# Kernel optimization log

Hardware: AMD Instinct MI355X
Metric: run time of the kernel (lower is better)

Reference implementation:

```python
import jax, jax.numpy as jnp
import numpy as np
from jax import lax

C = 256
HEADS = 8
HEAD_DIM = C // HEADS
B, H, W = 16, 32, 32
EPS = 1e-5


def conv3x3(x, w, b):
    # x: [B,C,H,W], w: [O,I,3,3]
    y = lax.conv_general_dilated(x, w, (1, 1), 'SAME',
                                 dimension_numbers=('NCHW', 'OIHW', 'NCHW'))
    return y + b[None, :, None, None]


def conv1x1(x, w, b):
    # w: [O,C]; pointwise conv as einsum
    return jnp.einsum('oc,bchw->bohw', w, x) + b[None, :, None, None]


def batchnorm(x, gamma, beta, mean, var):
    inv = gamma / jnp.sqrt(var + EPS)
    return x * inv[None, :, None, None] + (beta - mean * inv)[None, :, None, None]


def setup_inputs() -> dict:
    key = jax.random.key(0)
    ks = jax.random.split(key, 16)
    s3 = 1.0 / np.sqrt(C * 9)
    s1 = 1.0 / np.sqrt(C)
    return {
        'x': jax.random.normal(ks[0], (B, C, H, W), jnp.float32),
        'conv1_w': jax.random.normal(ks[1], (C, C, 3, 3), jnp.float32) * s3,
        'conv1_b': jnp.zeros((C,), jnp.float32),
        'bn1_gamma': jnp.ones((C,), jnp.float32),
        'bn1_beta': jnp.zeros((C,), jnp.float32),
        'bn1_mean': jax.random.normal(ks[2], (C,), jnp.float32) * 0.1,
        'bn1_var': jax.random.uniform(ks[3], (C,), jnp.float32, 0.5, 1.5),
        'conv2_w': jax.random.normal(ks[4], (C, C, 3, 3), jnp.float32) * s3,
        'conv2_b': jnp.zeros((C,), jnp.float32),
        'bn2_gamma': jnp.ones((C,), jnp.float32),
        'bn2_beta': jnp.zeros((C,), jnp.float32),
        'bn2_mean': jax.random.normal(ks[5], (C,), jnp.float32) * 0.1,
        'bn2_var': jax.random.uniform(ks[6], (C,), jnp.float32, 0.5, 1.5),
        'q_w': jax.random.normal(ks[7], (C, C), jnp.float32) * s1,
        'q_b': jnp.zeros((C,), jnp.float32),
        'k_w': jax.random.normal(ks[8], (C, C), jnp.float32) * s1,
        'k_b': jnp.zeros((C,), jnp.float32),
        'v_w': jax.random.normal(ks[9], (C, C), jnp.float32) * s1,
        'v_b': jnp.zeros((C,), jnp.float32),
        'out_w': jax.random.normal(ks[10], (C, C), jnp.float32) * s1,
        'out_b': jnp.zeros((C,), jnp.float32),
        'gate': jnp.asarray(0.1, jnp.float32),
    }


def reference(x, conv1_w, conv1_b, bn1_gamma, bn1_beta, bn1_mean, bn1_var,
              conv2_w, conv2_b, bn2_gamma, bn2_beta, bn2_mean, bn2_var,
              q_w, q_b, k_w, k_b, v_w, v_b, out_w, out_b, gate):
    b, c, h, w = x.shape
    n = h * w
    residual = x
    # conv residual path
    conv_out = jax.nn.relu(batchnorm(conv3x3(x, conv1_w, conv1_b),
                                     bn1_gamma, bn1_beta, bn1_mean, bn1_var))
    conv_out = batchnorm(conv3x3(conv_out, conv2_w, conv2_b),
                         bn2_gamma, bn2_beta, bn2_mean, bn2_var)
    # spatial multi-head attention (eval mode: dropout is identity)
    q = conv1x1(x, q_w, q_b).reshape(b, HEADS, HEAD_DIM, n)
    k = conv1x1(x, k_w, k_b).reshape(b, HEADS, HEAD_DIM, n)
    v = conv1x1(x, v_w, v_b).reshape(b, HEADS, HEAD_DIM, n)
    scores = jnp.einsum('bhdn,bhdm->bhnm', q, k) / np.sqrt(HEAD_DIM).astype(np.float32)
    attn = jax.nn.softmax(scores, axis=-1)  # [B,heads,N,N]
    attn_out = jnp.einsum('bhdm,bhnm->bhdn', v, attn).reshape(b, c, h, w)
    attn_out = conv1x1(attn_out, out_w, out_b)
    out = conv_out + jax.nn.sigmoid(gate) * attn_out + residual
    return jax.nn.relu(out)
```

## Files before the change

### kernel.cpp

```cpp
#include <hip/hip_runtime.h>
#include <hip/hip_bf16.h>

using bf16 = __hip_bfloat16;
typedef __attribute__((ext_vector_type(4))) float floatx4;
typedef __attribute__((ext_vector_type(8))) __bf16 bf16x8;
typedef __attribute__((ext_vector_type(4))) __bf16 bf16x4;
typedef __attribute__((ext_vector_type(8))) unsigned short ushort8;

__device__ __forceinline__ void prep_one(const float* __restrict__ src,
                                         bf16* __restrict__ dst, int idx, int ntaps)
{
    const int kk = idx & 31, o = (idx >> 5) & 255, kc = (idx >> 13) & 7, t = idx >> 16;
    dst[idx] = __float2bfloat16(src[(o * 256 + kc * 32 + kk) * ntaps + t]);
}

__global__ __launch_bounds__(256) void prep_all(
    const float* __restrict__ x,
    const float* __restrict__ w1, const float* __restrict__ w2,
    const float* __restrict__ qw, const float* __restrict__ kw,
    const float* __restrict__ vw, const float* __restrict__ ow,
    bf16* __restrict__ xT, bf16* __restrict__ w1f, bf16* __restrict__ w2f,
    bf16* __restrict__ qwf, bf16* __restrict__ kwf,
    bf16* __restrict__ vwf, bf16* __restrict__ owf)
{
    __shared__ float T[64][65];
    const int blk = blockIdx.x, tid = threadIdx.x;
    if (blk < 1024) {
        const int n0 = (blk & 15) * 64, c0 = ((blk >> 4) & 3) * 64, b = blk >> 6;
        #pragma unroll
        for (int it = 0; it < 4; ++it) {
            const int tau = tid + it * 256;
            const int c = tau >> 4, seg = tau & 15;
            const float4 vv = *(const float4*)&x[((b * 256 + c0 + c) << 10) + n0 + seg * 4];
            T[seg * 4 + 0][c] = vv.x; T[seg * 4 + 1][c] = vv.y;
            T[seg * 4 + 2][c] = vv.z; T[seg * 4 + 3][c] = vv.w;
        }
        __syncthreads();
        #pragma unroll
        for (int it = 0; it < 2; ++it) {
            const int tau = tid + it * 256;
            const int n = tau >> 3, seg = tau & 7;
            bf16x8 o8;
            #pragma unroll
            for (int q = 0; q < 8; ++q) o8[q] = (__bf16)T[n][seg * 8 + q];
            *(bf16x8*)&xT[(((b << 10) + n0 + n) << 8) + c0 + seg * 8] = o8;
        }
    } else if (blk < 2176) {
        const int base = (blk - 1024) * 256 + tid;
        #pragma unroll
        for (int k = 0; k < 4; ++k) {
            const int idx = base + k * 294912;
            if (idx < 589824) prep_one(w1, w1f, idx, 9);
            else              prep_one(w2, w2f, idx - 589824, 9);
        }
    } else {
        const int r = (blk - 2176) * 256 + tid;
        prep_one(qw, qwf, r, 1);
        prep_one(kw, kwf, r, 1);
        prep_one(vw, vwf, r, 1);
        prep_one(ow, owf, r, 1);
    }
}

template<int MODE, int NTAPS>
__global__ __launch_bounds__(256) void gemm_k(
    const bf16* __restrict__ Wf, const bf16* __restrict__ Act,
    const float* __restrict__ bias,
    const float* __restrict__ gam, const float* __restrict__ bet,
    const float* __restrict__ mu, const float* __restrict__ var,
    const float* __restrict__ c2, const float* __restrict__ resid,
    const float* __restrict__ gate,
    void* __restrict__ outp)
{
    __shared__ __align__(16) bf16 smem[(NTAPS == 9) ? (6 * 34 * 40) : (128 * 40)];

    const int bn = blockIdx.x, bo = blockIdx.y, b = blockIdx.z;
    const int tid = threadIdx.x;
    const int wave = tid >> 6, lane = tid & 63;
    const int quad = lane >> 4, l16 = lane & 15;
    const int wm = wave & 1, wn = wave >> 1;

    floatx4 acc[4][2] = {};

    for (int kc = 0; kc < 8; ++kc) {
        const int kg = kc * 32;
        __syncthreads();
        if (NTAPS == 9) {
            #pragma unroll
            for (int it = 0; it < 4; ++it) {
                const int tau = tid + it * 256;
                if (tau < 816) {
                    const int pair = tau >> 2, kseg = tau & 3;
                    const int yi = pair / 34, x34 = pair - yi * 34;
                    const int gy = bn * 4 - 1 + yi, gx = x34 - 1;
                    ushort8 val = {0, 0, 0, 0, 0, 0, 0, 0};
                    if (gy >= 0 && gy < 32 && gx >= 0 && gx < 32)
                        val = *(const ushort8*)&Act[(((b << 10) + (gy << 5) + gx) << 8) + kg + kseg * 8];
                    *(ushort8*)&smem[((yi * 34 + x34) * 40) + kseg * 8] = val;
                }
            }
        } else {
            #pragma unroll
            for (int it = 0; it < 2; ++it) {
                const int tau = tid + it * 256;
                const int row = tau >> 2, kseg = tau & 3;
                *(ushort8*)&smem[row * 40 + kseg * 8] =
                    *(const ushort8*)&Act[(((b << 10) + bn * 128 + row) << 8) + kg + kseg * 8];
            }
        }
        __syncthreads();

        #pragma unroll
        for (int t = 0; t < NTAPS; ++t) {
            const int dy = (NTAPS == 9) ? (t / 3 - 1) : 0;
            const int dx = (NTAPS == 9) ? (t % 3 - 1) : 0;
            bf16x8 af[4], wf[2];
            #pragma unroll
            for (int p = 0; p < 4; ++p) {
                const int m = wm * 64 + p * 16 + l16;
                if (NTAPS == 9) {
                    const int y = m >> 5, xx = m & 31;
                    af[p] = *(const bf16x8*)&smem[(((y + 1 + dy) * 34 + (xx + 1 + dx)) * 40) + quad * 8];
                } else {
                    af[p] = *(const bf16x8*)&smem[m * 40 + quad * 8];
                }
            }
            #pragma unroll
            for (int p = 0; p < 2; ++p) {
                const int ocl = wn * 32 + p * 16 + l16;
                wf[p] = *(const bf16x8*)&Wf[((((t * 8 + kc) << 8) + bo * 64 + ocl) << 5) + quad * 8];
            }
            #pragma unroll
            for (int i = 0; i < 4; ++i)
                #pragma unroll
                for (int j = 0; j < 2; ++j)
                    acc[i][j] = __builtin_amdgcn_mfma_f32_16x16x32_bf16(af[i], wf[j], acc[i][j], 0, 0, 0);
        }
    }

    float sg = 0.0f;
    if (MODE == 2) sg = 1.0f / (1.0f + __expf(-gate[0]));

    if constexpr (MODE == 0) {
        #pragma unroll
        for (int i = 0; i < 4; ++i)
            #pragma unroll
            for (int r = 0; r < 4; ++r) {
                const int n = bn * 128 + wm * 64 + i * 16 + quad * 4 + r;
                #pragma unroll
                for (int j = 0; j < 2; ++j) {
                    const int oc = bo * 64 + wn * 32 + j * 16 + l16;
                    const float inv = gam[oc] * rsqrtf(var[oc] + 1e-5f);
                    const float v = (acc[i][j][r] + bias[oc]) * inv + (bet[oc] - mu[oc] * inv);
                    ((bf16*)outp)[(((b << 10) + n) << 8) + oc] =
                        __float2bfloat16(v < 0.0f ? 0.0f : v);
                }
            }
    } else {
        #pragma unroll
        for (int i = 0; i < 4; ++i) {
            const int n0 = bn * 128 + wm * 64 + i * 16 + quad * 4;
            #pragma unroll
            for (int j = 0; j < 2; ++j) {
                const int oc = bo * 64 + wn * 32 + j * 16 + l16;
                const int idx0 = ((b * 256 + oc) << 10) + n0;
                const float bs = bias[oc];
                float4 o;
                if constexpr (MODE == 1) {
                    const float inv = gam[oc] * rsqrtf(var[oc] + 1e-5f);
                    const float sh = bet[oc] - mu[oc] * inv;
                    o.x = (acc[i][j][0] + bs) * inv + sh;
                    o.y = (acc[i][j][1] + bs) * inv + sh;
                    o.z = (acc[i][j][2] + bs) * inv + sh;
                    o.w = (acc[i][j][3] + bs) * inv + sh;
                } else {
                    const float4 cc = *(const float4*)&c2[idx0];
                    const float4 rr = *(const float4*)&resid[idx0];
                    o.x = cc.x + sg * (acc[i][j][0] + bs) + rr.x;
                    o.y = cc.y + sg * (acc[i][j][1] + bs) + rr.y;
                    o.z = cc.z + sg * (acc[i][j][2] + bs) + rr.z;
                    o.w = cc.w + sg * (acc[i][j][3] + bs) + rr.w;
                    o.x = o.x < 0.0f ? 0.0f : o.x;
                    o.y = o.y < 0.0f ? 0.0f : o.y;
                    o.z = o.z < 0.0f ? 0.0f : o.z;
                    o.w = o.w < 0.0f ? 0.0f : o.w;
                }
                *(float4*)&((float*)outp)[idx0] = o;
            }
        }
    }
}

__global__ __launch_bounds__(256) void qkv_k(
    const bf16* __restrict__ Wq, const bf16* __restrict__ Wk, const bf16* __restrict__ Wv,
    const bf16* __restrict__ Act,
    const float* __restrict__ bq, const float* __restrict__ bk, const float* __restrict__ bv,
    bf16* __restrict__ Oq, bf16* __restrict__ Ok, bf16* __restrict__ Ov, float qscale)
{
    __shared__ __align__(16) bf16 smem[128 * 40];
    const int bn = blockIdx.x, by = blockIdx.y, b = blockIdx.z;
    const int sel = by >> 2, bo = by & 3;
    const bf16* __restrict__ Wf = (sel == 0) ? Wq : (sel == 1) ? Wk : Wv;
    const float* __restrict__ bias = (sel == 0) ? bq : (sel == 1) ? bk : bv;
    const float scale = (sel == 0) ? qscale : 1.0f;

    const int tid = threadIdx.x;
    const int wave = tid >> 6, lane = tid & 63;
    const int quad = lane >> 4, l16 = lane & 15;
    const int wm = wave & 1, wn = wave >> 1;

    floatx4 acc[4][2] = {};

    for (int kc = 0; kc < 8; ++kc) {
        const int kg = kc * 32;
        __syncthreads();
        #pragma unroll
        for (int it = 0; it < 2; ++it) {
            const int tau = tid + it * 256;
            const int row = tau >> 2, kseg = tau & 3;
            *(ushort8*)&smem[row * 40 + kseg * 8] =
                *(const ushort8*)&Act[(((b << 10) + bn * 128 + row) << 8) + kg + kseg * 8];
        }
        __syncthreads();

        bf16x8 af[4], wf[2];
        #pragma unroll
        for (int p = 0; p < 4; ++p)
            af[p] = *(const bf16x8*)&smem[(wm * 64 + p * 16 + l16) * 40 + quad * 8];
        #pragma unroll
        for (int p = 0; p < 2; ++p) {
            const int ocl = wn * 32 + p * 16 + l16;
            wf[p] = *(const bf16x8*)&Wf[(((kc << 8) + bo * 64 + ocl) << 5) + quad * 8];
        }
        #pragma unroll
        for (int i = 0; i < 4; ++i)
            #pragma unroll
            for (int j = 0; j < 2; ++j)
                acc[i][j] = __builtin_amdgcn_mfma_f32_16x16x32_bf16(af[i], wf[j], acc[i][j], 0, 0, 0);
    }

    if (sel < 2) {
        bf16* __restrict__ outp = (sel == 0) ? Oq : Ok;
        #pragma unroll
        for (int i = 0; i < 4; ++i)
            #pragma unroll
            for (int r = 0; r < 4; ++r) {
                const int n = bn * 128 + wm * 64 + i * 16 + quad * 4 + r;
                #pragma unroll
                for (int j = 0; j < 2; ++j) {
                    const int oc = bo * 64 + wn * 32 + j * 16 + l16;
                    outp[(((b << 10) + n) << 8) + oc] =
                        __float2bfloat16((acc[i][j][r] + bias[oc]) * scale);
                }
            }
    } else {
        #pragma unroll
        for (int i = 0; i < 4; ++i) {
            const int n0 = bn * 128 + wm * 64 + i * 16 + quad * 4;
            #pragma unroll
            for (int j = 0; j < 2; ++j) {
                const int oc = bo * 64 + wn * 32 + j * 16 + l16;
                const float bs = bias[oc];
                bf16x4 o4;
                #pragma unroll
                for (int r = 0; r < 4; ++r) o4[r] = (__bf16)(acc[i][j][r] + bs);
                *(bf16x4*)&Ov[((b * 256 + oc) << 10) + n0] = o4;
            }
        }
    }
}

__global__ __launch_bounds__(256) void attn_kernel(
    const bf16* __restrict__ Q, const bf16* __restrict__ K,
    const bf16* __restrict__ V, bf16* __restrict__ O)
{
    __shared__ __align__(16) bf16 Pl[4][32][136];

    const int qb = blockIdx.x, h = blockIdx.y, b = blockIdx.z;
    const int tid = threadIdx.x;
    const int wave = tid >> 6, lane = tid & 63;
    const int quad = lane >> 4, l16 = lane & 15;

    const int qrow0 = (b << 10) + qb * 128 + wave * 32;

    bf16x8 qf[2];
    #pragma unroll
    for (int i = 0; i < 2; ++i)
        qf[i] = *(const bf16x8*)&Q[((qrow0 + i * 16 + l16) << 8) + h * 32 + quad * 8];

    float lp[2] = {0.0f, 0.0f};
    floatx4 oacc[2][2] = {};

    for (int kt = 0; kt < 8; ++kt) {
        const int krow0 = (b << 10) + kt * 128;
        bf16x8 kf[8];
        #pragma unroll
        for (int kb = 0; kb < 8; ++kb)
            kf[kb] = *(const bf16x8*)&K[((krow0 + kb * 16 + l16) << 8) + h * 32 + quad * 8];
        bf16x8 vb[2][4];
        #pragma unroll
        for (int jd = 0; jd < 2; ++jd)
            #pragma unroll
            for (int kk = 0; kk < 4; ++kk)
                vb[jd][kk] = *(const bf16x8*)&V[((b * 256 + h * 32 + jd * 16 + l16) << 10)
                                               + kt * 128 + kk * 32 + quad * 8];

        #pragma unroll
        for (int kb = 0; kb < 8; ++kb) {
            #pragma unroll
            for (int i = 0; i < 2; ++i) {
                floatx4 zz = {0.f, 0.f, 0.f, 0.f};
                floatx4 st = __builtin_amdgcn_mfma_f32_16x16x32_bf16(kf[kb], qf[i], zz, 0, 0, 0);
                const float e0 = __expf(st[0]), e1 = __expf(st[1]);
                const float e2 = __expf(st[2]), e3 = __expf(st[3]);
                lp[i] += (e0 + e1) + (e2 + e3);
                bf16x4 p4 = {(__bf16)e0, (__bf16)e1, (__bf16)e2, (__bf16)e3};
                *(bf16x4*)&Pl[wave][i * 16 + l16][kb * 16 + quad * 4] = p4;
            }
        }

        #pragma unroll
        for (int kk = 0; kk < 4; ++kk) {
            bf16x8 pf[2];
            #pragma unroll
            for (int i = 0; i < 2; ++i)
                pf[i] = *(const bf16x8*)&Pl[wave][i * 16 + l16][kk * 32 + quad * 8];
            #pragma unroll
            for (int jd = 0; jd < 2; ++jd)
                #pragma unroll
                for (int i = 0; i < 2; ++i)
                    oacc[jd][i] = __builtin_amdgcn_mfma_f32_16x16x32_bf16(
                        vb[jd][kk], pf[i], oacc[jd][i], 0, 0, 0);
        }
    }

    #pragma unroll
    for (int i = 0; i < 2; ++i) {
        float l = lp[i];
        l += __shfl_xor(l, 16, 64);
        l += __shfl_xor(l, 32, 64);
        const float inv = 1.0f / l;
        const int qn = qrow0 + i * 16 + l16;
        #pragma unroll
        for (int jd = 0; jd < 2; ++jd) {
            bf16x4 o4;
            #pragma unroll
            for (int r = 0; r < 4; ++r) o4[r] = (__bf16)(oacc[jd][i][r] * inv);
            *(bf16x4*)&O[((qn) << 8) + h * 32 + jd * 16 + quad * 4] = o4;
        }
    }
}

extern "C" void kernel_launch(void* const* d_in, const int* in_sizes, int n_in,
                              void* d_out, int out_size, void* d_ws, size_t ws_size,
                              hipStream_t stream)
{
    const float* x    = (const float*)d_in[0];
    const float* w1   = (const float*)d_in[1];
    const float* cb1  = (const float*)d_in[2];
    const float* g1   = (const float*)d_in[3];
    const float* be1  = (const float*)d_in[4];
    const float* mu1  = (const float*)d_in[5];
    const float* va1  = (const float*)d_in[6];
    const float* w2   = (const float*)d_in[7];
    const float* cb2  = (const float*)d_in[8];
    const float* g2   = (const float*)d_in[9];
    const float* be2  = (const float*)d_in[10];
    const float* mu2  = (const float*)d_in[11];
    const float* va2  = (const float*)d_in[12];
    const float* qw   = (const float*)d_in[13];
    const float* qb_  = (const float*)d_in[14];
    const float* kw   = (const float*)d_in[15];
    const float* kb_  = (const float*)d_in[16];
    const float* vw   = (const float*)d_in[17];
    const float* vb_  = (const float*)d_in[18];
    const float* ow   = (const float*)d_in[19];
    const float* ob_  = (const float*)d_in[20];
    const float* gate = (const float*)d_in[21];

    char* ws = (char*)d_ws;
    bf16*  xT    = (bf16*) (ws + 0);
    bf16*  y1T   = (bf16*) (ws + 8388608);
    bf16*  attnT = (bf16*) (ws + 8388608);
    float* c2    = (float*)(ws + 16777216);
    bf16*  qT    = (bf16*) (ws + 33554432);
    bf16*  kT    = (bf16*) (ws + 41943040);
    bf16*  vbuf  = (bf16*) (ws + 50331648);
    bf16*  w1f   = (bf16*) (ws + 58720256);
    bf16*  w2f   = (bf16*) (ws + 59899904);
    bf16*  qwf   = (bf16*) (ws + 61079552);
    bf16*  kwf   = (bf16*) (ws + 61210624);
    bf16*  vwf   = (bf16*) (ws + 61341696);
    bf16*  owf   = (bf16*) (ws + 61472768);

    dim3 blk(256, 1, 1);
    prep_all<<<dim3(2432), blk, 0, stream>>>(x, w1, w2, qw, kw, vw, ow,
                                             xT, w1f, w2f, qwf, kwf, vwf, owf);

    dim3 gg(8, 4, 16);
    gemm_k<0, 9><<<gg, blk, 0, stream>>>(w1f, xT, cb1, g1, be1, mu1, va1,
                                         nullptr, nullptr, nullptr, (void*)y1T);
    gemm_k<1, 9><<<gg, blk, 0, stream>>>(w2f, y1T, cb2, g2, be2, mu2, va2,
                                         nullptr, nullptr, nullptr, (void*)c2);
    qkv_k<<<dim3(8, 12, 16), blk, 0, stream>>>(qwf, kwf, vwf, xT, qb_, kb_, vb_,
                                               qT, kT, vbuf, 0.17677669529663687f);
    attn_kernel<<<dim3(8, 8, 16), blk, 0, stream>>>(qT, kT, vbuf, attnT);
    gemm_k<2, 1><<<gg, blk, 0, stream>>>(owf, attnT, ob_, nullptr, nullptr, nullptr, nullptr,
                                         c2, x, gate, d_out);

    (void)in_sizes; (void)n_in; (void)out_size; (void)ws_size;
}
```

Measured before the change: 275.6 us.

## Switch activations to channel-chunked layout and load MFMA operands directly from global

```diff
diff --git a/kernel.cpp b/kernel.cpp
--- a/kernel.cpp
+++ b/kernel.cpp
@@ -19,7 +19,7 @@
     const float* __restrict__ w1, const float* __restrict__ w2,
     const float* __restrict__ qw, const float* __restrict__ kw,
     const float* __restrict__ vw, const float* __restrict__ ow,
-    bf16* __restrict__ xT, bf16* __restrict__ w1f, bf16* __restrict__ w2f,
+    bf16* __restrict__ xk, bf16* __restrict__ w1f, bf16* __restrict__ w2f,
     bf16* __restrict__ qwf, bf16* __restrict__ kwf,
     bf16* __restrict__ vwf, bf16* __restrict__ owf)
 {
@@ -43,7 +43,8 @@
             bf16x8 o8;
             #pragma unroll
             for (int q = 0; q < 8; ++q) o8[q] = (__bf16)T[n][seg * 8 + q];
-            *(bf16x8*)&xT[(((b << 10) + n0 + n) << 8) + c0 + seg * 8] = o8;
+            const int c = c0 + seg * 8;
+            *(bf16x8*)&xk[((((b << 3) + (c >> 5)) << 10) + n0 + n) * 32 + (c & 31)] = o8;
         }
     } else if (blk < 2176) {
         const int base = (blk - 1024) * 256 + tid;
@@ -72,8 +73,6 @@
     const float* __restrict__ gate,
     void* __restrict__ outp)
 {
-    __shared__ __align__(16) bf16 smem[(NTAPS == 9) ? (6 * 34 * 40) : (128 * 40)];
-
     const int bn = blockIdx.x, bo = blockIdx.y, b = blockIdx.z;
     const int tid = threadIdx.x;
     const int wave = tid >> 6, lane = tid & 63;
@@ -83,33 +82,7 @@
     floatx4 acc[4][2] = {};
 
     for (int kc = 0; kc < 8; ++kc) {
-        const int kg = kc * 32;
-        __syncthreads();
-        if (NTAPS == 9) {
-            #pragma unroll
-            for (int it = 0; it < 4; ++it) {
-                const int tau = tid + it * 256;
-                if (tau < 816) {
-                    const int pair = tau >> 2, kseg = tau & 3;
-                    const int yi = pair / 34, x34 = pair - yi * 34;
-                    const int gy = bn * 4 - 1 + yi, gx = x34 - 1;
-                    ushort8 val = {0, 0, 0, 0, 0, 0, 0, 0};
-                    if (gy >= 0 && gy < 32 && gx >= 0 && gx < 32)
-                        val = *(const ushort8*)&Act[(((b << 10) + (gy << 5) + gx) << 8) + kg + kseg * 8];
-                    *(ushort8*)&smem[((yi * 34 + x34) * 40) + kseg * 8] = val;
-                }
-            }
-        } else {
-            #pragma unroll
-            for (int it = 0; it < 2; ++it) {
-                const int tau = tid + it * 256;
-                const int row = tau >> 2, kseg = tau & 3;
-                *(ushort8*)&smem[row * 40 + kseg * 8] =
-                    *(const ushort8*)&Act[(((b << 10) + bn * 128 + row) << 8) + kg + kseg * 8];
-            }
-        }
-        __syncthreads();
-
+        const bf16* __restrict__ actk = Act + ((((b << 3) + kc) << 10) << 5);
         #pragma unroll
         for (int t = 0; t < NTAPS; ++t) {
             const int dy = (NTAPS == 9) ? (t / 3 - 1) : 0;
@@ -119,10 +92,15 @@
             for (int p = 0; p < 4; ++p) {
                 const int m = wm * 64 + p * 16 + l16;
                 if (NTAPS == 9) {
-                    const int y = m >> 5, xx = m & 31;
-                    af[p] = *(const bf16x8*)&smem[(((y + 1 + dy) * 34 + (xx + 1 + dx)) * 40) + quad * 8];
+                    const int y = bn * 4 + (m >> 5) + dy;
+                    const int xx = (m & 31) + dx;
+                    const bool valid = (y >= 0) & (y < 32) & (xx >= 0) & (xx < 32);
+                    const int n = valid ? ((y << 5) + xx) : 0;
+                    bf16x8 v = {};
+                    if (valid) v = *(const bf16x8*)&actk[n * 32 + quad * 8];
+                    af[p] = v;
                 } else {
-                    af[p] = *(const bf16x8*)&smem[m * 40 + quad * 8];
+                    af[p] = *(const bf16x8*)&actk[(bn * 128 + m) * 32 + quad * 8];
                 }
             }
             #pragma unroll
@@ -142,6 +120,7 @@
     if (MODE == 2) sg = 1.0f / (1.0f + __expf(-gate[0]));
 
     if constexpr (MODE == 0) {
+        const int kc2 = bo * 2 + wn;
         #pragma unroll
         for (int i = 0; i < 4; ++i)
             #pragma unroll
@@ -152,7 +131,7 @@
                     const int oc = bo * 64 + wn * 32 + j * 16 + l16;
                     const float inv = gam[oc] * rsqrtf(var[oc] + 1e-5f);
                     const float v = (acc[i][j][r] + bias[oc]) * inv + (bet[oc] - mu[oc] * inv);
-                    ((bf16*)outp)[(((b << 10) + n) << 8) + oc] =
+                    ((bf16*)outp)[((((b << 3) + kc2) << 10) + n) * 32 + j * 16 + l16] =
                         __float2bfloat16(v < 0.0f ? 0.0f : v);
                 }
             }
@@ -197,7 +176,6 @@
     const float* __restrict__ bq, const float* __restrict__ bk, const float* __restrict__ bv,
     bf16* __restrict__ Oq, bf16* __restrict__ Ok, bf16* __restrict__ Ov, float qscale)
 {
-    __shared__ __align__(16) bf16 smem[128 * 40];
     const int bn = blockIdx.x, by = blockIdx.y, b = blockIdx.z;
     const int sel = by >> 2, bo = by & 3;
     const bf16* __restrict__ Wf = (sel == 0) ? Wq : (sel == 1) ? Wk : Wv;
@@ -212,21 +190,11 @@
     floatx4 acc[4][2] = {};
 
     for (int kc = 0; kc < 8; ++kc) {
-        const int kg = kc * 32;
-        __syncthreads();
-        #pragma unroll
-        for (int it = 0; it < 2; ++it) {
-            const int tau = tid + it * 256;
-            const int row = tau >> 2, kseg = tau & 3;
-            *(ushort8*)&smem[row * 40 + kseg * 8] =
-                *(const ushort8*)&Act[(((b << 10) + bn * 128 + row) << 8) + kg + kseg * 8];
-        }
-        __syncthreads();
-
+        const bf16* __restrict__ actk = Act + ((((b << 3) + kc) << 10) << 5);
         bf16x8 af[4], wf[2];
         #pragma unroll
         for (int p = 0; p < 4; ++p)
-            af[p] = *(const bf16x8*)&smem[(wm * 64 + p * 16 + l16) * 40 + quad * 8];
+            af[p] = *(const bf16x8*)&actk[(bn * 128 + wm * 64 + p * 16 + l16) * 32 + quad * 8];
         #pragma unroll
         for (int p = 0; p < 2; ++p) {
             const int ocl = wn * 32 + p * 16 + l16;
@@ -241,6 +209,7 @@
 
     if (sel < 2) {
         bf16* __restrict__ outp = (sel == 0) ? Oq : Ok;
+        const int h = bo * 2 + wn;
         #pragma unroll
         for (int i = 0; i < 4; ++i)
             #pragma unroll
@@ -249,7 +218,7 @@
                 #pragma unroll
                 for (int j = 0; j < 2; ++j) {
                     const int oc = bo * 64 + wn * 32 + j * 16 + l16;
-                    outp[(((b << 10) + n) << 8) + oc] =
+                    outp[((((b << 3) + h) << 10) + n) * 32 + j * 16 + l16] =
                         __float2bfloat16((acc[i][j][r] + bias[oc]) * scale);
                 }
             }
@@ -281,22 +250,23 @@
     const int wave = tid >> 6, lane = tid & 63;
     const int quad = lane >> 4, l16 = lane & 15;
 
-    const int qrow0 = (b << 10) + qb * 128 + wave * 32;
+    const bf16* __restrict__ Qh = Q + ((((b << 3) + h) << 10) << 5);
+    const bf16* __restrict__ Kh = K + ((((b << 3) + h) << 10) << 5);
+    const int qrow0 = qb * 128 + wave * 32;
 
     bf16x8 qf[2];
     #pragma unroll
     for (int i = 0; i < 2; ++i)
-        qf[i] = *(const bf16x8*)&Q[((qrow0 + i * 16 + l16) << 8) + h * 32 + quad * 8];
+        qf[i] = *(const bf16x8*)&Qh[(qrow0 + i * 16 + l16) * 32 + quad * 8];
 
     float lp[2] = {0.0f, 0.0f};
     floatx4 oacc[2][2] = {};
 
     for (int kt = 0; kt < 8; ++kt) {
-        const int krow0 = (b << 10) + kt * 128;
         bf16x8 kf[8];
         #pragma unroll
         for (int kb = 0; kb < 8; ++kb)
-            kf[kb] = *(const bf16x8*)&K[((krow0 + kb * 16 + l16) << 8) + h * 32 + quad * 8];
+            kf[kb] = *(const bf16x8*)&Kh[(kt * 128 + kb * 16 + l16) * 32 + quad * 8];
         bf16x8 vb[2][4];
         #pragma unroll
         for (int jd = 0; jd < 2; ++jd)
@@ -334,6 +304,7 @@
         }
     }
 
+    bf16* __restrict__ Oh = O + ((((b << 3) + h) << 10) << 5);
     #pragma unroll
     for (int i = 0; i < 2; ++i) {
         float l = lp[i];
@@ -346,7 +317,7 @@
             bf16x4 o4;
             #pragma unroll
             for (int r = 0; r < 4; ++r) o4[r] = (__bf16)(oacc[jd][i][r] * inv);
-            *(bf16x4*)&O[((qn) << 8) + h * 32 + jd * 16 + quad * 4] = o4;
+            *(bf16x4*)&Oh[qn * 32 + jd * 16 + quad * 4] = o4;
         }
     }
 }
@@ -379,9 +350,9 @@
     const float* gate = (const float*)d_in[21];
 
     char* ws = (char*)d_ws;
-    bf16*  xT    = (bf16*) (ws + 0);
-    bf16*  y1T   = (bf16*) (ws + 8388608);
-    bf16*  attnT = (bf16*) (ws + 8388608);
+    bf16*  xk    = (bf16*) (ws + 0);
+    bf16*  y1k   = (bf16*) (ws + 8388608);
+    bf16*  attnk = (bf16*) (ws + 8388608);
     float* c2    = (float*)(ws + 16777216);
     bf16*  qT    = (bf16*) (ws + 33554432);
     bf16*  kT    = (bf16*) (ws + 41943040);
@@ -395,17 +366,17 @@
 
     dim3 blk(256, 1, 1);
     prep_all<<<dim3(2432), blk, 0, stream>>>(x, w1, w2, qw, kw, vw, ow,
-                                             xT, w1f, w2f, qwf, kwf, vwf, owf);
+                                             xk, w1f, w2f, qwf, kwf, vwf, owf);
 
     dim3 gg(8, 4, 16);
-    gemm_k<0, 9><<<gg, blk, 0, stream>>>(w1f, xT, cb1, g1, be1, mu1, va1,
-                                         nullptr, nullptr, nullptr, (void*)y1T);
-    gemm_k<1, 9><<<gg, blk, 0, stream>>>(w2f, y1T, cb2, g2, be2, mu2, va2,
+    gemm_k<0, 9><<<gg, blk, 0, stream>>>(w1f, xk, cb1, g1, be1, mu1, va1,
+                                         nullptr, nullptr, nullptr, (void*)y1k);
+    gemm_k<1, 9><<<gg, blk, 0, stream>>>(w2f, y1k, cb2, g2, be2, mu2, va2,
                                          nullptr, nullptr, nullptr, (void*)c2);
-    qkv_k<<<dim3(8, 12, 16), blk, 0, stream>>>(qwf, kwf, vwf, xT, qb_, kb_, vb_,
+    qkv_k<<<dim3(8, 12, 16), blk, 0, stream>>>(qwf, kwf, vwf, xk, qb_, kb_, vb_,
                                                qT, kT, vbuf, 0.17677669529663687f);
-    attn_kernel<<<dim3(8, 8, 16), blk, 0, stream>>>(qT, kT, vbuf, attnT);
-    gemm_k<2, 1><<<gg, blk, 0, stream>>>(owf, attnT, ob_, nullptr, nullptr, nullptr, nullptr,
+    attn_kernel<<<dim3(8, 8, 16), blk, 0, stream>>>(qT, kT, vbuf, attnk);
+    gemm_k<2, 1><<<gg, blk, 0, stream>>>(owf, attnk, ob_, nullptr, nullptr, nullptr, nullptr,
                                          c2, x, gate, d_out);
 
     (void)in_sizes; (void)n_in; (void)out_size; (void)ws_size;
```

Result: slower. 304.3 us (+10.4%).
